# Kernel optimization log

Hardware: AMD Instinct MI355X
Metric: run time of the kernel (lower is better)

## Reference

```python
import jax, jax.numpy as jnp
import numpy as np

# SpikingConfig defaults
DECAY = 0.7
THRESHOLD = 1.0
K_WINNERS = 5
GAIN_UP = 1.5
GAIN_DOWN = 0.6
# reset_mode = 'soft'

L = 4096        # number of timesteps (flattened token ids)
V = 131072      # vocab size


def setup_inputs() -> dict:
    key = jax.random.key(0)
    k_ids, = jax.random.split(key, 1)
    token_ids = jax.random.randint(k_ids, (L,), 0, V, dtype=jnp.int64)
    potentials_init = jnp.zeros((V,), dtype=jnp.float32)  # module starts from zero potentials
    return {"token_ids": token_ids, "vocab_size": V, "potentials_init": potentials_init}


def reference(token_ids, vocab_size, potentials_init):
    ids = token_ids.reshape(-1)
    dtype = potentials_init.dtype
    decay = jnp.asarray(DECAY, dtype)
    thr = jnp.asarray(THRESHOLD, dtype)

    def step(carry, tid):
        pot, spk = carry
        pot = pot * decay                       # leaky decay over full vocab
        pot = pot.at[tid].add(jnp.asarray(1.0, dtype))  # bincount of a single token
        mask = pot >= thr                       # spike condition
        spk = spk + mask.astype(jnp.int32)
        pot = jnp.where(mask, pot - thr, pot)   # soft reset
        return (pot, spk), None

    init = (potentials_init, jnp.zeros((vocab_size,), jnp.int32))
    (pot, spk), _ = jax.lax.scan(step, init, ids)

    active = spk > 0
    # rank primarily by spike count, tie-break by residual potential
    values = spk.astype(jnp.float32) * 1e6 + pot.astype(jnp.float32)
    k = min(K_WINNERS, vocab_size)
    _, topk_idx = jax.lax.top_k(values, k)

    gains = jnp.where(active, jnp.asarray(GAIN_DOWN, dtype), jnp.asarray(1.0, dtype))
    gains = gains.at[topk_idx].set(jnp.asarray(GAIN_UP, dtype))
    # if nothing ever spiked, return all-ones (torch branch `if active.sum() > 0`)
    gains = jnp.where(jnp.any(active), gains, jnp.ones((vocab_size,), dtype))
    return gains
```

## Files before the change

### kernel.cpp

```cpp
#include <hip/hip_runtime.h>
#include <stdint.h>


typedef unsigned long long u64;

#define TB 1024
#define HSZ 8192
#define HMASK (HSZ - 1)
#define K_WIN 5

static __device__ __forceinline__ uint32_t hashf(uint32_t x) {
    return (x * 2654435761u) >> 19;
}
static __device__ __forceinline__ u64 u64max(u64 a, u64 b) { return a > b ? a : b; }

__global__ __launch_bounds__(TB) void kwta_kernel(const int* __restrict__ ids,
                                                  float* __restrict__ gains,
                                                  int L, int V) {
    __shared__ uint32_t sid[HSZ];
    __shared__ uint32_t scnt[HSZ];
    __shared__ u64 sWave[TB / 64];
    __shared__ u64 sWin;

    const int tid = threadIdx.x;
    const int lane = tid & 63, wid = tid >> 6;

    for (int i = tid; i < HSZ; i += TB) { sid[i] = 0u; scnt[i] = 0u; }
    __syncthreads();

    for (int i0 = tid * 4; i0 < L; i0 += TB * 4) {
        int idv[4];
        int n = 0;
        if (i0 + 3 < L) {
            int4 w = *reinterpret_cast<const int4*>(ids + i0);
            idv[0] = w.x; idv[1] = w.y; idv[2] = w.z; idv[3] = w.w;
            n = 4;
        } else {
            for (; i0 + n < L && n < 4; ++n) idv[n] = ids[i0 + n];
        }
        for (int j = 0; j < n; ++j) {
            uint32_t id = (uint32_t)idv[j];
            uint32_t s = hashf(id) & HMASK;
            for (;;) {
                uint32_t cur = sid[s];
                if (cur == id + 1u) { atomicAdd(&scnt[s], 1u); break; }
                if (cur == 0u) {
                    uint32_t got = atomicCAS(&sid[s], 0u, id + 1u);
                    if (got == 0u || got == id + 1u) { atomicAdd(&scnt[s], 1u); break; }
                }
                s = (s + 1) & HMASK;
            }
        }
    }

    const float4 one4 = make_float4(1.f, 1.f, 1.f, 1.f);
    float4* g4 = reinterpret_cast<float4*>(gains);
    const int V4 = V >> 2;
    for (int i = tid; i < V4; i += TB) g4[i] = one4;
    for (int i = (V4 << 2) + tid; i < V; i += TB) gains[i] = 1.0f;

    __syncthreads();

    u64 loc[K_WIN] = {0ull, 0ull, 0ull, 0ull, 0ull};
    for (int s = tid; s < HSZ; s += TB) {
        uint32_t idp1 = sid[s];
        if (idp1) {
            uint32_t id = idp1 - 1u;
            uint32_t c = scnt[s];
            gains[id] = 0.6f;
            u64 key = ((u64)c << 32) | (u64)(0xFFFFFFFFu - id);
            if (key > loc[K_WIN - 1]) {
                loc[K_WIN - 1] = key;
                for (int j = K_WIN - 1; j > 0 && loc[j] > loc[j - 1]; --j) {
                    u64 t = loc[j]; loc[j] = loc[j - 1]; loc[j - 1] = t;
                }
            }
        }
    }
    __syncthreads();

    int nz = 0;
    for (int it = 0; it < K_WIN; ++it) {
        u64 k = loc[0];
        for (int off = 32; off; off >>= 1) k = u64max(k, __shfl_xor(k, off));
        if (lane == 0) sWave[wid] = k;
        __syncthreads();
        if (tid == 0) {
            u64 w = sWave[0];
            for (int i = 1; i < TB / 64; ++i) w = u64max(w, sWave[i]);
            sWin = w;
        }
        __syncthreads();
        u64 w = sWin;
        if (w && loc[0] == w) {
            for (int j = 0; j < K_WIN - 1; ++j) loc[j] = loc[j + 1];
            loc[K_WIN - 1] = 0ull;
        }
        if (tid == 0 && w) {
            gains[0xFFFFFFFFu - (uint32_t)(w & 0xFFFFFFFFull)] = 1.5f;
            ++nz;
        }
        __syncthreads();
    }

    if (tid == 0 && nz < K_WIN) {
        int need = K_WIN - nz;
        for (uint32_t v = 0; need > 0 && v < (uint32_t)V; ++v) {
            uint32_t s = hashf(v) & HMASK;
            uint32_t c = 0u;
            for (;;) {
                uint32_t cur = sid[s];
                if (cur == 0u) break;
                if (cur == v + 1u) { c = scnt[s]; break; }
                s = (s + 1) & HMASK;
            }
            if (c == 0u) { gains[v] = 1.5f; --need; }
        }
    }
}

extern "C" void kernel_launch(void* const* d_in, const int* in_sizes, int n_in,
                              void* d_out, int out_size, void* d_ws, size_t ws_size,
                              hipStream_t stream) {
    const int* ids = (const int*)d_in[0];
    const int L = in_sizes[0];
    const int V = out_size;
    float* gains = (float*)d_out;
    kwta_kernel<<<1, TB, 0, stream>>>(ids, gains, L, V);
}
```

Before: 71.28 us.

## Split output over many blocks, each redundantly building the hash histogram

Launches one block per 1024-element slice of the vocab instead of a single block. Every block rebuilds the full token histogram in shared memory and then writes only its own slice of gains, using a per-element hash lookup instead of a full fill followed by scatter. The id and count are packed into a single 64-bit slot so one CAS both inserts and counts. This spreads the 512KB output write across the whole GPU, at the price of redundant histogram and top-k work in all 128 blocks.

```diff
diff --git a/kernel.cpp b/kernel.cpp
--- a/kernel.cpp
+++ b/kernel.cpp
@@ -5,6 +5,7 @@
 typedef unsigned long long u64;
 
 #define TB 1024
+#define SLICE 1024
 #define HSZ 8192
 #define HMASK (HSZ - 1)
 #define K_WIN 5
@@ -17,15 +18,16 @@
 __global__ __launch_bounds__(TB) void kwta_kernel(const int* __restrict__ ids,
                                                   float* __restrict__ gains,
                                                   int L, int V) {
-    __shared__ uint32_t sid[HSZ];
-    __shared__ uint32_t scnt[HSZ];
+    __shared__ u64 slot[HSZ];
     __shared__ u64 sWave[TB / 64];
     __shared__ u64 sWin;
+    __shared__ u64 sWinners[K_WIN];
 
     const int tid = threadIdx.x;
     const int lane = tid & 63, wid = tid >> 6;
+    const int base = blockIdx.x * SLICE;
 
-    for (int i = tid; i < HSZ; i += TB) { sid[i] = 0u; scnt[i] = 0u; }
+    for (int i = tid; i < HSZ; i += TB) slot[i] = 0ull;
     __syncthreads();
 
     for (int i0 = tid * 4; i0 < L; i0 += TB * 4) {
@@ -42,33 +44,42 @@
             uint32_t id = (uint32_t)idv[j];
             uint32_t s = hashf(id) & HMASK;
             for (;;) {
-                uint32_t cur = sid[s];
-                if (cur == id + 1u) { atomicAdd(&scnt[s], 1u); break; }
-                if (cur == 0u) {
-                    uint32_t got = atomicCAS(&sid[s], 0u, id + 1u);
-                    if (got == 0u || got == id + 1u) { atomicAdd(&scnt[s], 1u); break; }
+                u64 cur = slot[s];
+                uint32_t lo = (uint32_t)cur;
+                if (lo == id + 1u) { atomicAdd(&slot[s], 1ull << 32); break; }
+                if (lo == 0u) {
+                    u64 got = atomicCAS(&slot[s], 0ull, (1ull << 32) | (u64)(id + 1u));
+                    if (got == 0ull) break;
+                    if ((uint32_t)got == id + 1u) { atomicAdd(&slot[s], 1ull << 32); break; }
                 }
                 s = (s + 1) & HMASK;
             }
         }
     }
-
-    const float4 one4 = make_float4(1.f, 1.f, 1.f, 1.f);
-    float4* g4 = reinterpret_cast<float4*>(gains);
-    const int V4 = V >> 2;
-    for (int i = tid; i < V4; i += TB) g4[i] = one4;
-    for (int i = (V4 << 2) + tid; i < V; i += TB) gains[i] = 1.0f;
-
     __syncthreads();
 
+    {
+        int v = base + tid;
+        if (v < V) {
+            uint32_t s = hashf((uint32_t)v) & HMASK;
+            uint32_t c = 0u;
+            for (;;) {
+                u64 cur = slot[s];
+                uint32_t lo = (uint32_t)cur;
+                if (lo == (uint32_t)v + 1u) { c = (uint32_t)(cur >> 32); break; }
+                if (lo == 0u) break;
+                s = (s + 1) & HMASK;
+            }
+            gains[v] = c ? 0.6f : 1.0f;
+        }
+    }
+
     u64 loc[K_WIN] = {0ull, 0ull, 0ull, 0ull, 0ull};
-    for (int s = tid; s < HSZ; s += TB) {
-        uint32_t idp1 = sid[s];
-        if (idp1) {
-            uint32_t id = idp1 - 1u;
-            uint32_t c = scnt[s];
-            gains[id] = 0.6f;
-            u64 key = ((u64)c << 32) | (u64)(0xFFFFFFFFu - id);
+    for (int i = tid; i < HSZ; i += TB) {
+        u64 cur = slot[i];
+        if (cur) {
+            uint32_t id = (uint32_t)cur - 1u;
+            u64 key = (cur & 0xFFFFFFFF00000000ull) | (u64)(0xFFFFFFFFu - id);
             if (key > loc[K_WIN - 1]) {
                 loc[K_WIN - 1] = key;
                 for (int j = K_WIN - 1; j > 0 && loc[j] > loc[j - 1]; --j) {
@@ -77,7 +88,6 @@
             }
         }
     }
-    __syncthreads();
 
     int nz = 0;
     for (int it = 0; it < K_WIN; ++it) {
@@ -89,6 +99,7 @@
             u64 w = sWave[0];
             for (int i = 1; i < TB / 64; ++i) w = u64max(w, sWave[i]);
             sWin = w;
+            sWinners[it] = w;
         }
         __syncthreads();
         u64 w = sWin;
@@ -96,11 +107,15 @@
             for (int j = 0; j < K_WIN - 1; ++j) loc[j] = loc[j + 1];
             loc[K_WIN - 1] = 0ull;
         }
-        if (tid == 0 && w) {
-            gains[0xFFFFFFFFu - (uint32_t)(w & 0xFFFFFFFFull)] = 1.5f;
-            ++nz;
-        }
+        if (w) ++nz;
         __syncthreads();
+    }
+
+    if (tid < K_WIN && tid < nz) {
+        u64 w = sWinners[tid];
+        uint32_t idx = 0xFFFFFFFFu - (uint32_t)(w & 0xFFFFFFFFull);
+        if ((int)idx >= base && (int)idx < base + SLICE && (int)idx < V)
+            gains[idx] = 1.5f;
     }
 
     if (tid == 0 && nz < K_WIN) {
@@ -109,12 +124,16 @@
             uint32_t s = hashf(v) & HMASK;
             uint32_t c = 0u;
             for (;;) {
-                uint32_t cur = sid[s];
-                if (cur == 0u) break;
-                if (cur == v + 1u) { c = scnt[s]; break; }
+                u64 cur = slot[s];
+                uint32_t lo = (uint32_t)cur;
+                if (lo == 0u) break;
+                if (lo == v + 1u) { c = (uint32_t)(cur >> 32); break; }
                 s = (s + 1) & HMASK;
             }
-            if (c == 0u) { gains[v] = 1.5f; --need; }
+            if (c == 0u) {
+                if ((int)v >= base && (int)v < base + SLICE) gains[v] = 1.5f;
+                --need;
+            }
         }
     }
 }
@@ -126,5 +145,6 @@
     const int L = in_sizes[0];
     const int V = out_size;
     float* gains = (float*)d_out;
-    kwta_kernel<<<1, TB, 0, stream>>>(ids, gains, L, V);
+    const int nblk = (V + SLICE - 1) / SLICE;
+    kwta_kernel<<<nblk, TB, 0, stream>>>(ids, gains, L, V);
 }
```

New measurement: 77.62 us. 8.9% more time.
